# Optimization experiments

Hardware: AMD Instinct MI355X
Metric: run time of the kernel (lower is better)

Reference implementation:

```python
import jax, jax.numpy as jnp
import numpy as np

N_NODES = 50000
N_EDGES = 1600000
N_GRAPHS = 64
DIMS = [3, 256, 256, 256]  # in -> hidden -> hidden -> output
BN_EPS = 1e-5


def setup_inputs() -> dict:
    key = jax.random.key(0)
    ks = jax.random.split(key, 32)
    inp = {}
    inp['x'] = jax.random.normal(ks[0], (N_NODES, DIMS[0]), dtype=jnp.float32)
    inp['edge_index'] = jax.random.randint(ks[1], (2, N_EDGES), 0, N_NODES, dtype=jnp.int64)
    inp['batch'] = jnp.sort(jax.random.randint(ks[2], (N_NODES,), 0, N_GRAPHS, dtype=jnp.int64))
    k = 3
    for i in range(3):
        fi, fo = DIMS[i], DIMS[i + 1]
        inp[f'W{i}'] = jax.random.normal(ks[k], (fi, fo), dtype=jnp.float32) / np.sqrt(fi); k += 1
        inp[f'b{i}'] = jnp.zeros((fo,), dtype=jnp.float32)
        inp[f'g{i}'] = jnp.ones((fo,), dtype=jnp.float32)       # BN weight
        inp[f'be{i}'] = jnp.zeros((fo,), dtype=jnp.float32)     # BN bias
        inp[f'm{i}'] = 0.1 * jax.random.normal(ks[k], (fo,), dtype=jnp.float32); k += 1  # running mean
        inp[f'v{i}'] = jax.random.uniform(ks[k], (fo,), dtype=jnp.float32) + 0.5; k += 1  # running var
    return inp


def _gcn_norm(edge_index, n_nodes):
    # add self-loops, compute symmetric normalization (PyG GCNConv gcn_norm)
    loops = jnp.arange(n_nodes, dtype=edge_index.dtype)
    src = jnp.concatenate([edge_index[0], loops])
    dst = jnp.concatenate([edge_index[1], loops])
    deg = jax.ops.segment_sum(jnp.ones_like(dst, dtype=jnp.float32), dst, num_segments=n_nodes)
    dinv = jnp.where(deg > 0, jax.lax.rsqrt(deg), 0.0)
    norm = dinv[src] * dinv[dst]  # [E+N]
    return src, dst, norm


def _gcn_conv(x, W, b, src, dst, norm, n_nodes):
    h = x @ W                                 # [N, out]
    msg = h[src] * norm[:, None]              # gather + edge weight
    out = jax.ops.segment_sum(msg, dst, num_segments=n_nodes)  # scatter-add
    return out + b


def _bn_eval(x, g, be, m, v):
    return (x - m) * jax.lax.rsqrt(v + BN_EPS) * g + be


def _denan(x):
    return jnp.where(jnp.isnan(x), 0.0, x)


def reference(x, edge_index, batch,
              W0, b0, g0, be0, m0, v0,
              W1, b1, g1, be1, m1, v1,
              W2, b2, g2, be2, m2, v2):
    n = x.shape[0]
    src, dst, norm = _gcn_norm(edge_index, n)
    params = [(W0, b0, g0, be0, m0, v0), (W1, b1, g1, be1, m1, v1), (W2, b2, g2, be2, m2, v2)]
    h = x
    for i, (W, b, g, be, m, v) in enumerate(params):
        h = _gcn_conv(h, W, b, src, dst, norm, n)
        h = _bn_eval(h, g, be, m, v)
        if i < 2:
            h = jax.nn.relu(h)  # dropout is identity in eval mode
        h = _denan(h)
    # global_mean_pool over batch segments
    sums = jax.ops.segment_sum(h, batch, num_segments=N_GRAPHS)
    cnt = jax.ops.segment_sum(jnp.ones((n,), dtype=h.dtype), batch, num_segments=N_GRAPHS)
    out = sums / jnp.maximum(cnt, 1.0)[:, None]
    return _denan(out)
```

## Files before the change

### kernel.cpp

```cpp
#include <hip/hip_runtime.h>

#define NFEAT 256
#define BN_EPSF 1e-5f
#define CH_J 512
#define ELLW 96
#define BSH 7
#define PBKT 392
#define PCAP 4608
#define PEDG 4992
#define W1_SCALE 8.0f
#define Y_DESCALE 0.125f

typedef __attribute__((ext_vector_type(8))) short bf16x8;
typedef __attribute__((ext_vector_type(4))) float f32x4;
typedef __attribute__((ext_vector_type(2))) float f32x2;

__device__ __forceinline__ unsigned short f2bf(float f) {
    union { float f; unsigned u; } v; v.f = f;
    unsigned r = v.u + 0x7fffu + ((v.u >> 16) & 1u);
    return (unsigned short)(r >> 16);
}
__device__ __forceinline__ float bf2f(unsigned short h) {
    union { unsigned u; float f; } v; v.u = ((unsigned)h) << 16;
    return v.f;
}


__global__ __launch_bounds__(256) void k_part(const int* __restrict__ src, const int* __restrict__ dst,
                                              int* __restrict__ curD, int* __restrict__ curS,
                                              unsigned* __restrict__ partD, unsigned* __restrict__ partS, int E) {
    __shared__ int cD[PBKT], cS[PBKT], bD[PBKT], bS[PBKT];
    __shared__ int2 eds[PEDG];
    for (int t = threadIdx.x; t < PBKT; t += 256) { cD[t] = 0; cS[t] = 0; }
    __syncthreads();
    int e0 = blockIdx.x * PEDG;
    int ne = min(E - e0, PEDG);
    for (int i = threadIdx.x; i < ne; i += 256) {
        int2 e; e.x = src[e0 + i]; e.y = dst[e0 + i];
        eds[i] = e;
        atomicAdd(&cD[e.y >> BSH], 1);
        atomicAdd(&cS[e.x >> BSH], 1);
    }
    __syncthreads();
    for (int t = threadIdx.x; t < PBKT; t += 256) {
        bD[t] = cD[t] ? atomicAdd(&curD[t], cD[t]) : 0;
        bS[t] = cS[t] ? atomicAdd(&curS[t], cS[t]) : 0;
        cD[t] = 0; cS[t] = 0;
    }
    __syncthreads();
    for (int i = threadIdx.x; i < ne; i += 256) {
        int2 e = eds[i];
        int b1 = e.y >> BSH;
        int p1 = bD[b1] + atomicAdd(&cD[b1], 1);
        if (p1 < PCAP) partD[(size_t)b1 * PCAP + p1] = ((unsigned)(e.y & 127) << 16) | (unsigned)e.x;
        int b2 = e.x >> BSH;
        int p2 = bS[b2] + atomicAdd(&cS[b2], 1);
        if (p2 < PCAP) partS[(size_t)b2 * PCAP + p2] = ((unsigned)(e.x & 127) << 16) | (unsigned)e.y;
    }
}

__global__ __launch_bounds__(256) void k_prep(const float* __restrict__ W,
                                              unsigned char* __restrict__ Wt_hi, unsigned char* __restrict__ Wt_lo,
                                              const float* __restrict__ x, float4* __restrict__ x4, int N) {
    if (blockIdx.x < 256) {
        int n = blockIdx.x, k = threadIdx.x;
        float w8 = W[k * 256 + n] * W1_SCALE;
        int ph = __builtin_amdgcn_cvt_pk_fp8_f32(w8, w8, 0, false);
        f32x2 dec = __builtin_amdgcn_cvt_pk_f32_fp8(ph, false);
        int pl = __builtin_amdgcn_cvt_pk_fp8_f32(w8 - dec[0], w8 - dec[0], 0, false);
        Wt_hi[n * 256 + k] = (unsigned char)(ph & 0xff);
        Wt_lo[n * 256 + k] = (unsigned char)(pl & 0xff);
    } else {
        int i = (blockIdx.x - 256) * 256 + threadIdx.x;
        if (i < N) {
            float4 r; r.x = x[i * 3 + 0]; r.y = x[i * 3 + 1]; r.z = x[i * 3 + 2]; r.w = 0.f;
            x4[i] = r;
        }
    }
}

__global__ __launch_bounds__(256) void k_buildIn(const unsigned* __restrict__ partD, const int* __restrict__ curD,
                                                 const int* __restrict__ batch,
                                                 unsigned short* __restrict__ ell_in, int* __restrict__ cnt,
                                                 float* __restrict__ dinv, float2* __restrict__ pack, int N) {
    __shared__ int rows[128][ELLW];
    __shared__ int cur[128];
    int b = blockIdx.x;
    if (threadIdx.x < 128) cur[threadIdx.x] = 0;
    __syncthreads();
    int lo = b << BSH;
    int ne = min(curD[b], PCAP);
    const unsigned* seg = partD + (size_t)b * PCAP;
    for (int i = threadIdx.x; i < ne; i += 256) {
        unsigned u = seg[i];
        int r = u >> 16;
        int pos = atomicAdd(&cur[r], 1);
        if (pos < ELLW) rows[r][pos] = (int)(u & 0xFFFFu);
    }
    __syncthreads();
    const int Q = ELLW / 8;
    for (int idx = threadIdx.x; idx < 128 * Q; idx += 256) {
        int r = idx / Q, q = idx % Q;
        if (lo + r < N) {
            unsigned short tmp[8];
#pragma unroll
            for (int j = 0; j < 8; j++) tmp[j] = (unsigned short)rows[r][q * 8 + j];
            *(uint4*)(ell_in + (size_t)(lo + r) * ELLW + q * 8) = *(const uint4*)tmp;
        }
    }
    if (threadIdx.x < 128) {
        int node = lo + threadIdx.x;
        if (node < N) {
            int c = cur[threadIdx.x];
            cnt[node] = c;
            float d = rsqrtf((float)(min(c, ELLW) + 1));
            dinv[node] = d;
            float2 pk; pk.x = d; pk.y = __int_as_float(batch[node]);
            pack[node] = pk;
        }
    }
}

__global__ __launch_bounds__(256) void k_buildCt(const unsigned* __restrict__ partS, const int* __restrict__ curS,
                                                 const float2* __restrict__ pack,
                                                 unsigned short* __restrict__ ct_hi,
                                                 unsigned short* __restrict__ ct_lo,
                                                 int N, int N_pad) {
    __shared__ float ct[128][65];
    __shared__ float dv[128];
    int b = blockIdx.x;
    for (int idx = threadIdx.x; idx < 128 * 65; idx += 256) (&ct[0][0])[idx] = 0.f;
    __syncthreads();
    int lo = b << BSH;
    int ne = min(curS[b], PCAP);
    const unsigned* seg = partS + (size_t)b * PCAP;
    for (int i = threadIdx.x; i < ne; i += 256) {
        unsigned u = seg[i];
        float2 pk = pack[u & 0xFFFFu];
        atomicAdd(&ct[u >> 16][__float_as_int(pk.y)], pk.x);
    }
    __syncthreads();
    if (threadIdx.x < 128) {
        int node = lo + threadIdx.x;
        if (node < N) {
            float2 ps = pack[node];
            dv[threadIdx.x] = ps.x;
            ct[threadIdx.x][__float_as_int(ps.y)] += ps.x;
        } else dv[threadIdx.x] = 0.f;
    }
    __syncthreads();
    int g = threadIdx.x >> 2, js = (threadIdx.x & 3) * 32;
    unsigned short hv[32], lv[32];
#pragma unroll
    for (int j = 0; j < 32; j++) {
        float val = dv[js + j] * ct[js + j][g];
        unsigned short h = f2bf(val);
        hv[j] = h;
        lv[j] = f2bf(val - bf2f(h));
    }
    size_t basep = (size_t)g * N_pad + lo + js;
#pragma unroll
    for (int j = 0; j < 32; j += 8) {
        *(uint4*)(ct_hi + basep + j) = *(const uint4*)&hv[j];
        *(uint4*)(ct_lo + basep + j) = *(const uint4*)&lv[j];
    }
}


__global__ __launch_bounds__(256) void k_l0(const float4* __restrict__ x4, const unsigned short* __restrict__ ell_in,
                                            const int* __restrict__ cnt, const float* __restrict__ dinv,
                                            const float* __restrict__ W, const float* __restrict__ b,
                                            const float* __restrict__ g, const float* __restrict__ be,
                                            const float* __restrict__ m, const float* __restrict__ v,
                                            unsigned char* __restrict__ h8, int N) {
    int wv = threadIdx.x >> 6, lane = threadIdx.x & 63;
    int node = blockIdx.x * 4 + wv;
    int c4 = lane * 4;
    if (node >= N) {
        *(unsigned*)(h8 + (size_t)node * NFEAT + c4) = 0u;
        return;
    }
    float dvn = dinv[node];
    int len = min(cnt[node], ELLW);
    const unsigned short* nb = ell_in + (size_t)node * ELLW;
    float a0 = 0.f, a1 = 0.f, a2 = 0.f;
    for (int e = lane; e < len; e += 64) {
        int s = nb[e];
        float4 xv = x4[s];
        float w = dinv[s] * dvn;
        a0 += w * xv.x;
        a1 += w * xv.y;
        a2 += w * xv.z;
    }
#pragma unroll
    for (int off = 32; off; off >>= 1) {
        a0 += __shfl_xor(a0, off);
        a1 += __shfl_xor(a1, off);
        a2 += __shfl_xor(a2, off);
    }
    float4 xs = x4[node];
    float wself = dvn * dvn;
    a0 += wself * xs.x;
    a1 += wself * xs.y;
    a2 += wself * xs.z;
    float4 w0 = *(const float4*)(W + c4);
    float4 w1 = *(const float4*)(W + NFEAT + c4);
    float4 w2 = *(const float4*)(W + 2 * NFEAT + c4);
    float4 bb = *(const float4*)(b + c4);
    float4 gg = *(const float4*)(g + c4);
    float4 ee = *(const float4*)(be + c4);
    float4 mm = *(const float4*)(m + c4);
    float4 vv = *(const float4*)(v + c4);
    float r0 = ((a0 * w0.x + a1 * w1.x + a2 * w2.x) + bb.x - mm.x) * rsqrtf(vv.x + BN_EPSF) * gg.x + ee.x;
    float r1 = ((a0 * w0.y + a1 * w1.y + a2 * w2.y) + bb.y - mm.y) * rsqrtf(vv.y + BN_EPSF) * gg.y + ee.y;
    float r2 = ((a0 * w0.z + a1 * w1.z + a2 * w2.z) + bb.z - mm.z) * rsqrtf(vv.z + BN_EPSF) * gg.z + ee.z;
    float r3 = ((a0 * w0.w + a1 * w1.w + a2 * w2.w) + bb.w - mm.w) * rsqrtf(vv.w + BN_EPSF) * gg.w + ee.w;
    r0 = fmaxf(r0, 0.f); r1 = fmaxf(r1, 0.f); r2 = fmaxf(r2, 0.f); r3 = fmaxf(r3, 0.f);
    int p01 = __builtin_amdgcn_cvt_pk_fp8_f32(r0, r1, 0, false);
    int p23 = __builtin_amdgcn_cvt_pk_fp8_f32(r2, r3, 0, false);
    unsigned pk = (unsigned)(p01 & 0xffff) | ((unsigned)(p23 & 0xffff) << 16);
    *(unsigned*)(h8 + (size_t)node * NFEAT + c4) = pk;
}


__global__ __launch_bounds__(256) void k_mm_mfma(const unsigned char* __restrict__ A8,
                                                 const unsigned char* __restrict__ Bh,
                                                 const unsigned char* __restrict__ Bl,
                                                 unsigned char* __restrict__ C8) {
    __shared__ __align__(16) unsigned char As[4][128][8];
    __shared__ __align__(16) unsigned char Bhs[4][128][8];
    __shared__ __align__(16) unsigned char Bls[4][128][8];
    int bm = blockIdx.x * 128, bn = blockIdx.y * 128;
    int tid = threadIdx.x;
    int lane = tid & 63, wave = tid >> 6;
    int wm = (wave & 1) * 64, wn = (wave >> 1) * 64;
    int lrow = lane & 15, lk = lane >> 4;
    f32x4 acc[4][4] = {};

    for (int k0 = 0; k0 < 256; k0 += 32) {
#pragma unroll
        for (int i = 0; i < 2; i++) {
            int idx = tid + 256 * i;
            int ch = idx & 3, row = idx >> 2;
            *(uint2*)(&As[ch][row][0])  = *(const uint2*)(A8 + (size_t)(bm + row) * 256 + k0 + ch * 8);
            *(uint2*)(&Bhs[ch][row][0]) = *(const uint2*)(Bh + (size_t)(bn + row) * 256 + k0 + ch * 8);
            *(uint2*)(&Bls[ch][row][0]) = *(const uint2*)(Bl + (size_t)(bn + row) * 256 + k0 + ch * 8);
        }
        __syncthreads();
        long af[4], bh[4], bl[4];
#pragma unroll
        for (int r = 0; r < 4; r++) af[r] = *(const long*)(&As[lk][wm + r * 16 + lrow][0]);
#pragma unroll
        for (int c = 0; c < 4; c++) {
            bh[c] = *(const long*)(&Bhs[lk][wn + c * 16 + lrow][0]);
            bl[c] = *(const long*)(&Bls[lk][wn + c * 16 + lrow][0]);
        }
#pragma unroll
        for (int r = 0; r < 4; r++)
#pragma unroll
            for (int c = 0; c < 4; c++) {
                acc[r][c] = __builtin_amdgcn_mfma_f32_16x16x32_fp8_fp8(af[r], bh[c], acc[r][c], 0, 0, 0);
                acc[r][c] = __builtin_amdgcn_mfma_f32_16x16x32_fp8_fp8(af[r], bl[c], acc[r][c], 0, 0, 0);
            }
        __syncthreads();
    }

#pragma unroll
    for (int r = 0; r < 4; r++) {
#pragma unroll
        for (int reg = 0; reg < 4; reg++) {
            int grow = bm + wm + r * 16 + lk * 4 + reg;
            int p01 = __builtin_amdgcn_cvt_pk_fp8_f32(acc[r][0][reg], acc[r][1][reg], 0, false);
            int p23 = __builtin_amdgcn_cvt_pk_fp8_f32(acc[r][2][reg], acc[r][3][reg], 0, false);
            size_t base = (size_t)grow * 256 + bn + wn + lrow;
            C8[base]      = (unsigned char)(p01 & 0xff);
            C8[base + 16] = (unsigned char)((p01 >> 8) & 0xff);
            C8[base + 32] = (unsigned char)(p23 & 0xff);
            C8[base + 48] = (unsigned char)((p23 >> 8) & 0xff);
        }
    }
}


template <bool RELU>
__global__ __launch_bounds__(64) void k_agg256b(const unsigned char* __restrict__ t,
                                                const unsigned short* __restrict__ ell_in,
                                                const int* __restrict__ cnt,
                                                const float* __restrict__ dinv,
                                                const float* __restrict__ b, const float* __restrict__ g,
                                                const float* __restrict__ be, const float* __restrict__ m,
                                                const float* __restrict__ v, unsigned short* __restrict__ out, int N) {
    __shared__ int s_idx[64];
    __shared__ float s_w[64];
    int node = blockIdx.x;
    int c4 = threadIdx.x * 4;
    if (node >= N) {
        ushort4 z = {0, 0, 0, 0};
        *(ushort4*)(out + (size_t)node * NFEAT + c4) = z;
        return;
    }
    float dv = dinv[node];
    float a0, a1, a2, a3;
    {
        unsigned u = *(const unsigned*)(t + (size_t)node * NFEAT + c4);
        f32x2 flo = __builtin_amdgcn_cvt_pk_f32_fp8(u, false);
        f32x2 fhi = __builtin_amdgcn_cvt_pk_f32_fp8(u, true);
        float w = dv * dv;
        a0 = w * flo[0]; a1 = w * flo[1]; a2 = w * fhi[0]; a3 = w * fhi[1];
    }
    int len = min(cnt[node], ELLW);
    const unsigned short* nb = ell_in + (size_t)node * ELLW;
    for (int base = 0; base < len; base += 64) {
        int chunk = min(64, len - base);
        if ((int)threadIdx.x < chunk) {
            int s = nb[base + threadIdx.x];
            s_idx[threadIdx.x] = s;
            s_w[threadIdx.x] = dinv[s] * dv;
        }
        __syncthreads();
        int j = 0;
        for (; j + 4 <= chunk; j += 4) {
            unsigned u0 = *(const unsigned*)(t + (size_t)s_idx[j + 0] * NFEAT + c4);
            unsigned u1 = *(const unsigned*)(t + (size_t)s_idx[j + 1] * NFEAT + c4);
            unsigned u2 = *(const unsigned*)(t + (size_t)s_idx[j + 2] * NFEAT + c4);
            unsigned u3 = *(const unsigned*)(t + (size_t)s_idx[j + 3] * NFEAT + c4);
            float w0 = s_w[j + 0], w1 = s_w[j + 1], w2 = s_w[j + 2], w3 = s_w[j + 3];
            f32x2 l0 = __builtin_amdgcn_cvt_pk_f32_fp8(u0, false), h0 = __builtin_amdgcn_cvt_pk_f32_fp8(u0, true);
            f32x2 l1 = __builtin_amdgcn_cvt_pk_f32_fp8(u1, false), h1 = __builtin_amdgcn_cvt_pk_f32_fp8(u1, true);
            f32x2 l2 = __builtin_amdgcn_cvt_pk_f32_fp8(u2, false), h2 = __builtin_amdgcn_cvt_pk_f32_fp8(u2, true);
            f32x2 l3 = __builtin_amdgcn_cvt_pk_f32_fp8(u3, false), h3 = __builtin_amdgcn_cvt_pk_f32_fp8(u3, true);
            a0 += w0 * l0[0]; a1 += w0 * l0[1]; a2 += w0 * h0[0]; a3 += w0 * h0[1];
            a0 += w1 * l1[0]; a1 += w1 * l1[1]; a2 += w1 * h1[0]; a3 += w1 * h1[1];
            a0 += w2 * l2[0]; a1 += w2 * l2[1]; a2 += w2 * h2[0]; a3 += w2 * h2[1];
            a0 += w3 * l3[0]; a1 += w3 * l3[1]; a2 += w3 * h3[0]; a3 += w3 * h3[1];
        }
        for (; j < chunk; j++) {
            unsigned u = *(const unsigned*)(t + (size_t)s_idx[j] * NFEAT + c4);
            float w = s_w[j];
            f32x2 flo = __builtin_amdgcn_cvt_pk_f32_fp8(u, false);
            f32x2 fhi = __builtin_amdgcn_cvt_pk_f32_fp8(u, true);
            a0 += w * flo[0]; a1 += w * flo[1]; a2 += w * fhi[0]; a3 += w * fhi[1];
        }
        __syncthreads();
    }
    a0 *= Y_DESCALE; a1 *= Y_DESCALE; a2 *= Y_DESCALE; a3 *= Y_DESCALE;
    float4 bb = *(const float4*)(b + c4);
    float4 gg = *(const float4*)(g + c4);
    float4 ee = *(const float4*)(be + c4);
    float4 mm = *(const float4*)(m + c4);
    float4 vv = *(const float4*)(v + c4);
    float r0 = (a0 + bb.x - mm.x) * rsqrtf(vv.x + BN_EPSF) * gg.x + ee.x;
    float r1 = (a1 + bb.y - mm.y) * rsqrtf(vv.y + BN_EPSF) * gg.y + ee.y;
    float r2 = (a2 + bb.z - mm.z) * rsqrtf(vv.z + BN_EPSF) * gg.z + ee.z;
    float r3 = (a3 + bb.w - mm.w) * rsqrtf(vv.w + BN_EPSF) * gg.w + ee.w;
    if (RELU) { r0 = fmaxf(r0, 0.f); r1 = fmaxf(r1, 0.f); r2 = fmaxf(r2, 0.f); r3 = fmaxf(r3, 0.f); }
    ushort4 o; o.x = f2bf(r0); o.y = f2bf(r1); o.z = f2bf(r2); o.w = f2bf(r3);
    *(ushort4*)(out + (size_t)node * NFEAT + c4) = o;
}


__global__ __launch_bounds__(256) void k_cgemm(const unsigned short* __restrict__ Y,
                                               const unsigned short* __restrict__ ct_hi,
                                               const unsigned short* __restrict__ ct_lo,
                                               float* __restrict__ P, int N_pad) {
    __shared__ __align__(16) unsigned short s_hi[64 * 40];
    __shared__ __align__(16) unsigned short s_lo[64 * 40];
    int tid = threadIdx.x;
    int lane = tid & 63, wv = tid >> 6;
    int lc = lane & 15, q = lane >> 4;
    int cbase = blockIdx.y * 64 + wv * 16;
    int j0 = blockIdx.x * CH_J;
    int sg = tid >> 2, sj8 = (tid & 3) * 8;
    f32x4 acc[4] = {};

    for (int ks = 0; ks < CH_J; ks += 32) {
        size_t cbs = (size_t)sg * N_pad + j0 + ks + sj8;
        *(uint4*)(&s_hi[sg * 40 + sj8]) = *(const uint4*)(ct_hi + cbs);
        *(uint4*)(&s_lo[sg * 40 + sj8]) = *(const uint4*)(ct_lo + cbs);
        __syncthreads();
        const unsigned short* yp = Y + (size_t)(j0 + ks + q * 8) * 256 + cbase + lc;
        bf16x8 a;
#pragma unroll
        for (int jj = 0; jj < 8; jj++) a[jj] = (short)yp[(size_t)jj * 256];
#pragma unroll
        for (int nt = 0; nt < 4; nt++) {
            bf16x8 bh = *(const bf16x8*)(&s_hi[(nt * 16 + lc) * 40 + q * 8]);
            bf16x8 bl = *(const bf16x8*)(&s_lo[(nt * 16 + lc) * 40 + q * 8]);
            acc[nt] = __builtin_amdgcn_mfma_f32_16x16x32_bf16(a, bh, acc[nt], 0, 0, 0);
            acc[nt] = __builtin_amdgcn_mfma_f32_16x16x32_bf16(a, bl, acc[nt], 0, 0, 0);
        }
        __syncthreads();
    }
    float* pp = P + (size_t)blockIdx.x * 64 * 256;
#pragma unroll
    for (int nt = 0; nt < 4; nt++) {
        int g = nt * 16 + lc;
#pragma unroll
        for (int reg = 0; reg < 4; reg++) {
            int c = cbase + q * 4 + reg;
            pp[(size_t)c * 64 + g] = acc[nt][reg];
        }
    }
}

__global__ __launch_bounds__(64) void k_redP(const float* __restrict__ P,
                                             float* __restrict__ pooled, int nch) {
    int c = blockIdx.x;
    int g = threadIdx.x;
    float acc = 0.f;
    const float* pp = P + (size_t)c * 64 + g;
    for (int ch = 0; ch < nch; ch++) acc += pp[(size_t)ch * 64 * 256];
    pooled[(size_t)g * 256 + c] = acc;
}

__global__ __launch_bounds__(256) void k_out(const float* __restrict__ pooled,
                                             const float* __restrict__ W2,
                                             const int* __restrict__ batch,
                                             const float* __restrict__ b, const float* __restrict__ gw,
                                             const float* __restrict__ be, const float* __restrict__ m,
                                             const float* __restrict__ v,
                                             float* __restrict__ out, int N) {
    __shared__ float s_pool[256];
    __shared__ int s_cnt;
    int g = blockIdx.x;
    int c = threadIdx.x;
    s_pool[c] = pooled[(size_t)g * 256 + c];
    if (threadIdx.x == 0) {
        int lo = 0, hi = N;
        while (lo < hi) { int mid = (lo + hi) >> 1; if (batch[mid] < g) lo = mid + 1; else hi = mid; }
        int st = lo;
        lo = 0; hi = N;
        while (lo < hi) { int mid = (lo + hi) >> 1; if (batch[mid] < g + 1) lo = mid + 1; else hi = mid; }
        s_cnt = lo - st;
    }
    __syncthreads();
    float dot = 0.f;
    for (int k = 0; k < 256; k += 4) {
        float4 pk = *(const float4*)(s_pool + k);
        dot += pk.x * W2[(k + 0) * 256 + c];
        dot += pk.y * W2[(k + 1) * 256 + c];
        dot += pk.z * W2[(k + 2) * 256 + c];
        dot += pk.w * W2[(k + 3) * 256 + c];
    }
    float r = 0.f;
    int cntg = s_cnt;
    if (cntg > 0) {
        float mean = dot / (float)cntg + b[c];
        r = (mean - m[c]) * rsqrtf(v[c] + BN_EPSF) * gw[c] + be[c];
    }
    out[g * 256 + c] = r;
}


static inline size_t align_up(size_t x, size_t a) { return (x + a - 1) & ~(a - 1); }

extern "C" void kernel_launch(void* const* d_in, const int* in_sizes, int n_in,
                              void* d_out, int out_size, void* d_ws, size_t ws_size,
                              hipStream_t stream) {
    const float* x = (const float*)d_in[0];
    const int* edge_index = (const int*)d_in[1];
    const int* batch = (const int*)d_in[2];

    const int N = in_sizes[2];
    const int E = in_sizes[1] / 2;
    const int NCH = (N + CH_J - 1) / CH_J;
    const int N_pad = NCH * CH_J;

    const int* e_src = edge_index;
    const int* e_dst = edge_index + E;

    const float* W[3]; const float* bP[3]; const float* gP[3];
    const float* beP[3]; const float* mP[3]; const float* vP[3];
    for (int i = 0; i < 3; i++) {
        W[i]  = (const float*)d_in[3 + 6 * i + 0];
        bP[i] = (const float*)d_in[3 + 6 * i + 1];
        gP[i] = (const float*)d_in[3 + 6 * i + 2];
        beP[i]= (const float*)d_in[3 + 6 * i + 3];
        mP[i] = (const float*)d_in[3 + 6 * i + 4];
        vP[i] = (const float*)d_in[3 + 6 * i + 5];
    }

    char* ws = (char*)d_ws;
    size_t off = 0;
    auto carve = [&](size_t bytes) { void* p = ws + off; off = align_up(off + bytes, 256); return p; };
    int*   curD     = (int*)  carve((size_t)2 * PBKT * 4);
    int*   curS     = curD + PBKT;
    int*   cnt      = (int*)  carve((size_t)N * 4);
    float* dinv     = (float*)carve((size_t)N * 4);
    float2* pack    = (float2*)carve((size_t)N * 8);
    float4* x4      = (float4*)carve((size_t)N * 16);
    unsigned* partD = (unsigned*)carve((size_t)PBKT * PCAP * 4);
    unsigned* partS = (unsigned*)carve((size_t)PBKT * PCAP * 4);
    unsigned short* ell_in = (unsigned short*)carve((size_t)N * ELLW * 2);
    unsigned short* bufA = (unsigned short*)carve((size_t)N_pad * NFEAT * 2);
    unsigned char*  bufA0 = (unsigned char*)carve((size_t)N_pad * NFEAT);
    unsigned char*  bufY = (unsigned char*)carve((size_t)N_pad * NFEAT);
    unsigned char*  Wt_hi = (unsigned char*)carve((size_t)NFEAT * NFEAT);
    unsigned char*  Wt_lo = (unsigned char*)carve((size_t)NFEAT * NFEAT);
    unsigned short* ct_hi = (unsigned short*)carve((size_t)N_pad * 64 * 2);
    unsigned short* ct_lo = (unsigned short*)carve((size_t)N_pad * 64 * 2);
    float* partials = (float*)carve((size_t)NCH * 64 * 256 * 4);
    float* pooled   = (float*)carve((size_t)64 * 256 * 4);
    (void)ws_size;

    hipMemsetAsync(curD, 0, (size_t)2 * PBKT * 4, stream);

    const int BS = 256;
    k_part<<<(E + PEDG - 1) / PEDG, BS, 0, stream>>>(e_src, e_dst, curD, curS, partD, partS, E);
    k_prep<<<256 + (N + BS - 1) / BS, BS, 0, stream>>>(W[1], Wt_hi, Wt_lo, x, x4, N);
    k_buildIn<<<PBKT, BS, 0, stream>>>(partD, curD, batch, ell_in, cnt, dinv, pack, N);
    k_buildCt<<<PBKT, BS, 0, stream>>>(partS, curS, pack, ct_hi, ct_lo, N, N_pad);

    k_l0<<<N_pad / 4, BS, 0, stream>>>(x4, ell_in, cnt, dinv, W[0],
                                       bP[0], gP[0], beP[0], mP[0], vP[0], bufA0, N);

    dim3 mmGrid((N + 127) / 128, 2);
    k_mm_mfma<<<mmGrid, 256, 0, stream>>>(bufA0, Wt_hi, Wt_lo, bufY);
    k_agg256b<true><<<N_pad, 64, 0, stream>>>(bufY, ell_in, cnt, dinv,
                                              bP[1], gP[1], beP[1], mP[1], vP[1], bufA, N);

    dim3 cgGrid(NCH, 4);
    k_cgemm<<<cgGrid, 256, 0, stream>>>(bufA, ct_hi, ct_lo, partials, N_pad);
    k_redP<<<256, 64, 0, stream>>>(partials, pooled, NCH);
    k_out<<<64, 256, 0, stream>>>(pooled, W[2], batch, bP[2], gP[2], beP[2], mP[2], vP[2],
                                  (float*)d_out, N);
}
```

Measured before the change: 324.9 us.

## Pack four nodes per block in aggregation with scalar indices and packed FMA

The layer-1 aggregation kernel now runs four wavefronts per 256-thread block, one node each, instead of one 64-thread block per node. Neighbor index and weight are packed as int2 in shared memory and broadcast through readfirstlane, so the gather addresses come from scalar registers. The inner loop is unrolled to 8 gathers with packed f32x2 FMAs. This cuts block-launch overhead and exposes more memory-level parallelism. In exchange, all four waves loop to the block's maximum chunk count with block-wide barriers, so a short-degree node waits on its longest sibling.

New measurement: 333.3 us. +2.6%, slower.

```diff
diff --git a/kernel.cpp b/kernel.cpp
--- a/kernel.cpp
+++ b/kernel.cpp
@@ -282,68 +282,116 @@
 }
 
 
+__device__ __forceinline__ f32x2 pk_fma2(f32x2 x, float w, f32x2 acc) {
+    f32x2 ww = {w, w};
+    return x * ww + acc;
+}
+
 template <bool RELU>
-__global__ __launch_bounds__(64) void k_agg256b(const unsigned char* __restrict__ t,
-                                                const unsigned short* __restrict__ ell_in,
-                                                const int* __restrict__ cnt,
-                                                const float* __restrict__ dinv,
-                                                const float* __restrict__ b, const float* __restrict__ g,
-                                                const float* __restrict__ be, const float* __restrict__ m,
-                                                const float* __restrict__ v, unsigned short* __restrict__ out, int N) {
-    __shared__ int s_idx[64];
-    __shared__ float s_w[64];
-    int node = blockIdx.x;
-    int c4 = threadIdx.x * 4;
-    if (node >= N) {
-        ushort4 z = {0, 0, 0, 0};
-        *(ushort4*)(out + (size_t)node * NFEAT + c4) = z;
-        return;
-    }
-    float dv = dinv[node];
-    float a0, a1, a2, a3;
-    {
+__global__ __launch_bounds__(256) void k_agg256b(const unsigned char* __restrict__ t,
+                                                 const unsigned short* __restrict__ ell_in,
+                                                 const int* __restrict__ cnt,
+                                                 const float* __restrict__ dinv,
+                                                 const float* __restrict__ b, const float* __restrict__ g,
+                                                 const float* __restrict__ be, const float* __restrict__ m,
+                                                 const float* __restrict__ v, unsigned short* __restrict__ out, int N) {
+    __shared__ int2 s_sw[4][64];
+    __shared__ int s_nch;
+    int wv = threadIdx.x >> 6, lane = threadIdx.x & 63;
+    int node = blockIdx.x * 4 + wv;
+    int c4 = lane * 4;
+    bool valid = node < N;
+    float dv = valid ? dinv[node] : 0.f;
+    int len = valid ? min(cnt[node], ELLW) : 0;
+    if (threadIdx.x == 0) s_nch = 0;
+    __syncthreads();
+    if (lane == 0 && len > 0) atomicMax(&s_nch, (len + 63) >> 6);
+
+    f32x2 aLo = {0.f, 0.f}, aHi = {0.f, 0.f};
+    if (valid) {
         unsigned u = *(const unsigned*)(t + (size_t)node * NFEAT + c4);
         f32x2 flo = __builtin_amdgcn_cvt_pk_f32_fp8(u, false);
         f32x2 fhi = __builtin_amdgcn_cvt_pk_f32_fp8(u, true);
         float w = dv * dv;
-        a0 = w * flo[0]; a1 = w * flo[1]; a2 = w * fhi[0]; a3 = w * fhi[1];
-    }
-    int len = min(cnt[node], ELLW);
+        aLo = pk_fma2(flo, w, aLo);
+        aHi = pk_fma2(fhi, w, aHi);
+    }
+    __syncthreads();
+    int nch = s_nch;
     const unsigned short* nb = ell_in + (size_t)node * ELLW;
-    for (int base = 0; base < len; base += 64) {
-        int chunk = min(64, len - base);
-        if ((int)threadIdx.x < chunk) {
-            int s = nb[base + threadIdx.x];
-            s_idx[threadIdx.x] = s;
-            s_w[threadIdx.x] = dinv[s] * dv;
+
+    for (int it = 0; it < nch; ++it) {
+        int base = it << 6;
+        int chunk = min(len - base, 64);
+        if (lane < chunk) {
+            int s = nb[base + lane];
+            int2 p; p.x = s; p.y = __float_as_int(dinv[s] * dv);
+            s_sw[wv][lane] = p;
         }
         __syncthreads();
         int j = 0;
-        for (; j + 4 <= chunk; j += 4) {
-            unsigned u0 = *(const unsigned*)(t + (size_t)s_idx[j + 0] * NFEAT + c4);
-            unsigned u1 = *(const unsigned*)(t + (size_t)s_idx[j + 1] * NFEAT + c4);
-            unsigned u2 = *(const unsigned*)(t + (size_t)s_idx[j + 2] * NFEAT + c4);
-            unsigned u3 = *(const unsigned*)(t + (size_t)s_idx[j + 3] * NFEAT + c4);
-            float w0 = s_w[j + 0], w1 = s_w[j + 1], w2 = s_w[j + 2], w3 = s_w[j + 3];
-            f32x2 l0 = __builtin_amdgcn_cvt_pk_f32_fp8(u0, false), h0 = __builtin_amdgcn_cvt_pk_f32_fp8(u0, true);
-            f32x2 l1 = __builtin_amdgcn_cvt_pk_f32_fp8(u1, false), h1 = __builtin_amdgcn_cvt_pk_f32_fp8(u1, true);
-            f32x2 l2 = __builtin_amdgcn_cvt_pk_f32_fp8(u2, false), h2 = __builtin_amdgcn_cvt_pk_f32_fp8(u2, true);
-            f32x2 l3 = __builtin_amdgcn_cvt_pk_f32_fp8(u3, false), h3 = __builtin_amdgcn_cvt_pk_f32_fp8(u3, true);
-            a0 += w0 * l0[0]; a1 += w0 * l0[1]; a2 += w0 * h0[0]; a3 += w0 * h0[1];
-            a0 += w1 * l1[0]; a1 += w1 * l1[1]; a2 += w1 * h1[0]; a3 += w1 * h1[1];
-            a0 += w2 * l2[0]; a1 += w2 * l2[1]; a2 += w2 * h2[0]; a3 += w2 * h2[1];
-            a0 += w3 * l3[0]; a1 += w3 * l3[1]; a2 += w3 * h3[0]; a3 += w3 * h3[1];
+        for (; j + 8 <= chunk; j += 8) {
+            int2 p0 = s_sw[wv][j + 0], p1 = s_sw[wv][j + 1], p2 = s_sw[wv][j + 2], p3 = s_sw[wv][j + 3];
+            int2 p4 = s_sw[wv][j + 4], p5 = s_sw[wv][j + 5], p6 = s_sw[wv][j + 6], p7 = s_sw[wv][j + 7];
+            int s0 = __builtin_amdgcn_readfirstlane(p0.x);
+            int s1 = __builtin_amdgcn_readfirstlane(p1.x);
+            int s2 = __builtin_amdgcn_readfirstlane(p2.x);
+            int s3 = __builtin_amdgcn_readfirstlane(p3.x);
+            int s4 = __builtin_amdgcn_readfirstlane(p4.x);
+            int s5 = __builtin_amdgcn_readfirstlane(p5.x);
+            int s6 = __builtin_amdgcn_readfirstlane(p6.x);
+            int s7 = __builtin_amdgcn_readfirstlane(p7.x);
+            unsigned u0 = *(const unsigned*)(t + (size_t)s0 * NFEAT + c4);
+            unsigned u1 = *(const unsigned*)(t + (size_t)s1 * NFEAT + c4);
+            unsigned u2 = *(const unsigned*)(t + (size_t)s2 * NFEAT + c4);
+            unsigned u3 = *(const unsigned*)(t + (size_t)s3 * NFEAT + c4);
+            unsigned u4 = *(const unsigned*)(t + (size_t)s4 * NFEAT + c4);
+            unsigned u5 = *(const unsigned*)(t + (size_t)s5 * NFEAT + c4);
+            unsigned u6 = *(const unsigned*)(t + (size_t)s6 * NFEAT + c4);
+            unsigned u7 = *(const unsigned*)(t + (size_t)s7 * NFEAT + c4);
+            float w0 = __uint_as_float(__builtin_amdgcn_readfirstlane(p0.y));
+            float w1 = __uint_as_float(__builtin_amdgcn_readfirstlane(p1.y));
+            float w2 = __uint_as_float(__builtin_amdgcn_readfirstlane(p2.y));
+            float w3 = __uint_as_float(__builtin_amdgcn_readfirstlane(p3.y));
+            float w4 = __uint_as_float(__builtin_amdgcn_readfirstlane(p4.y));
+            float w5 = __uint_as_float(__builtin_amdgcn_readfirstlane(p5.y));
+            float w6 = __uint_as_float(__builtin_amdgcn_readfirstlane(p6.y));
+            float w7 = __uint_as_float(__builtin_amdgcn_readfirstlane(p7.y));
+            aLo = pk_fma2(__builtin_amdgcn_cvt_pk_f32_fp8(u0, false), w0, aLo);
+            aHi = pk_fma2(__builtin_amdgcn_cvt_pk_f32_fp8(u0, true),  w0, aHi);
+            aLo = pk_fma2(__builtin_amdgcn_cvt_pk_f32_fp8(u1, false), w1, aLo);
+            aHi = pk_fma2(__builtin_amdgcn_cvt_pk_f32_fp8(u1, true),  w1, aHi);
+            aLo = pk_fma2(__builtin_amdgcn_cvt_pk_f32_fp8(u2, false), w2, aLo);
+            aHi = pk_fma2(__builtin_amdgcn_cvt_pk_f32_fp8(u2, true),  w2, aHi);
+            aLo = pk_fma2(__builtin_amdgcn_cvt_pk_f32_fp8(u3, false), w3, aLo);
+            aHi = pk_fma2(__builtin_amdgcn_cvt_pk_f32_fp8(u3, true),  w3, aHi);
+            aLo = pk_fma2(__builtin_amdgcn_cvt_pk_f32_fp8(u4, false), w4, aLo);
+            aHi = pk_fma2(__builtin_amdgcn_cvt_pk_f32_fp8(u4, true),  w4, aHi);
+            aLo = pk_fma2(__builtin_amdgcn_cvt_pk_f32_fp8(u5, false), w5, aLo);
+            aHi = pk_fma2(__builtin_amdgcn_cvt_pk_f32_fp8(u5, true),  w5, aHi);
+            aLo = pk_fma2(__builtin_amdgcn_cvt_pk_f32_fp8(u6, false), w6, aLo);
+            aHi = pk_fma2(__builtin_amdgcn_cvt_pk_f32_fp8(u6, true),  w6, aHi);
+            aLo = pk_fma2(__builtin_amdgcn_cvt_pk_f32_fp8(u7, false), w7, aLo);
+            aHi = pk_fma2(__builtin_amdgcn_cvt_pk_f32_fp8(u7, true),  w7, aHi);
         }
         for (; j < chunk; j++) {
-            unsigned u = *(const unsigned*)(t + (size_t)s_idx[j] * NFEAT + c4);
-            float w = s_w[j];
-            f32x2 flo = __builtin_amdgcn_cvt_pk_f32_fp8(u, false);
-            f32x2 fhi = __builtin_amdgcn_cvt_pk_f32_fp8(u, true);
-            a0 += w * flo[0]; a1 += w * flo[1]; a2 += w * fhi[0]; a3 += w * fhi[1];
+            int2 p = s_sw[wv][j];
+            int s = __builtin_amdgcn_readfirstlane(p.x);
+            float w = __uint_as_float(__builtin_amdgcn_readfirstlane(p.y));
+            unsigned u = *(const unsigned*)(t + (size_t)s * NFEAT + c4);
+            aLo = pk_fma2(__builtin_amdgcn_cvt_pk_f32_fp8(u, false), w, aLo);
+            aHi = pk_fma2(__builtin_amdgcn_cvt_pk_f32_fp8(u, true),  w, aHi);
         }
         __syncthreads();
     }
-    a0 *= Y_DESCALE; a1 *= Y_DESCALE; a2 *= Y_DESCALE; a3 *= Y_DESCALE;
+
+    if (!valid) {
+        ushort4 z = {0, 0, 0, 0};
+        *(ushort4*)(out + (size_t)node * NFEAT + c4) = z;
+        return;
+    }
+    float a0 = aLo[0] * Y_DESCALE, a1 = aLo[1] * Y_DESCALE;
+    float a2 = aHi[0] * Y_DESCALE, a3 = aHi[1] * Y_DESCALE;
     float4 bb = *(const float4*)(b + c4);
     float4 gg = *(const float4*)(g + c4);
     float4 ee = *(const float4*)(be + c4);
@@ -516,8 +564,8 @@
 
     dim3 mmGrid((N + 127) / 128, 2);
     k_mm_mfma<<<mmGrid, 256, 0, stream>>>(bufA0, Wt_hi, Wt_lo, bufY);
-    k_agg256b<true><<<N_pad, 64, 0, stream>>>(bufY, ell_in, cnt, dinv,
-                                              bP[1], gP[1], beP[1], mP[1], vP[1], bufA, N);
+    k_agg256b<true><<<N_pad / 4, 256, 0, stream>>>(bufY, ell_in, cnt, dinv,
+                                                   bP[1], gP[1], beP[1], mP[1], vP[1], bufA, N);
 
     dim3 cgGrid(NCH, 4);
     k_cgemm<<<cgGrid, 256, 0, stream>>>(bufA, ct_hi, ct_lo, partials, N_pad);
```

## Fuse independent kernels, fold source dinv into GEMM epilogue, merge pooling reduction

Applied to the files above, without the earlier changes.

Merges the edge partitioning and weight/x prep into one launch, and the transpose-count build and layer-0 aggregation into another, using block-index ranges. The GEMM epilogue now pre-scales each row by its dinv, so the layer-1 aggregation only sums fp8 neighbor rows without per-edge weight lookups. The aggregation loop is unrolled by 8 with 32-bit offsets. The partials reduction is folded into k_out with vectorised partial stores, which removes several launches. Pre-scaling before fp8 quantisation changes rounding, and the kernel now mixes heterogeneous block types.

Result: faster. 315.2 us (-3.0%).

```diff
diff --git a/kernel.cpp b/kernel.cpp
--- a/kernel.cpp
+++ b/kernel.cpp
@@ -26,11 +26,34 @@
 }
 
 
-__global__ __launch_bounds__(256) void k_part(const int* __restrict__ src, const int* __restrict__ dst,
-                                              int* __restrict__ curD, int* __restrict__ curS,
-                                              unsigned* __restrict__ partD, unsigned* __restrict__ partS, int E) {
+__global__ __launch_bounds__(256) void k_part_prep(const int* __restrict__ src, const int* __restrict__ dst,
+                                                   int* __restrict__ curD, int* __restrict__ curS,
+                                                   unsigned* __restrict__ partD, unsigned* __restrict__ partS,
+                                                   int E, int NPB,
+                                                   const float* __restrict__ W1,
+                                                   unsigned char* __restrict__ Wt_hi, unsigned char* __restrict__ Wt_lo,
+                                                   const float* __restrict__ x, float4* __restrict__ x4, int N) {
     __shared__ int cD[PBKT], cS[PBKT], bD[PBKT], bS[PBKT];
     __shared__ int2 eds[PEDG];
+    if ((int)blockIdx.x >= NPB) {
+        int bx = (int)blockIdx.x - NPB;
+        if (bx < 256) {
+            int n = bx, k = threadIdx.x;
+            float w8 = W1[k * 256 + n] * W1_SCALE;
+            int ph = __builtin_amdgcn_cvt_pk_fp8_f32(w8, w8, 0, false);
+            f32x2 dec = __builtin_amdgcn_cvt_pk_f32_fp8(ph, false);
+            int pl = __builtin_amdgcn_cvt_pk_fp8_f32(w8 - dec[0], w8 - dec[0], 0, false);
+            Wt_hi[n * 256 + k] = (unsigned char)(ph & 0xff);
+            Wt_lo[n * 256 + k] = (unsigned char)(pl & 0xff);
+        } else {
+            int i = (bx - 256) * 256 + threadIdx.x;
+            if (i < N) {
+                float4 r; r.x = x[i * 3 + 0]; r.y = x[i * 3 + 1]; r.z = x[i * 3 + 2]; r.w = 0.f;
+                x4[i] = r;
+            }
+        }
+        return;
+    }
     for (int t = threadIdx.x; t < PBKT; t += 256) { cD[t] = 0; cS[t] = 0; }
     __syncthreads();
     int e0 = blockIdx.x * PEDG;
@@ -56,26 +79,6 @@
         int b2 = e.x >> BSH;
         int p2 = bS[b2] + atomicAdd(&cS[b2], 1);
         if (p2 < PCAP) partS[(size_t)b2 * PCAP + p2] = ((unsigned)(e.x & 127) << 16) | (unsigned)e.y;
-    }
-}
-
-__global__ __launch_bounds__(256) void k_prep(const float* __restrict__ W,
-                                              unsigned char* __restrict__ Wt_hi, unsigned char* __restrict__ Wt_lo,
-                                              const float* __restrict__ x, float4* __restrict__ x4, int N) {
-    if (blockIdx.x < 256) {
-        int n = blockIdx.x, k = threadIdx.x;
-        float w8 = W[k * 256 + n] * W1_SCALE;
-        int ph = __builtin_amdgcn_cvt_pk_fp8_f32(w8, w8, 0, false);
-        f32x2 dec = __builtin_amdgcn_cvt_pk_f32_fp8(ph, false);
-        int pl = __builtin_amdgcn_cvt_pk_fp8_f32(w8 - dec[0], w8 - dec[0], 0, false);
-        Wt_hi[n * 256 + k] = (unsigned char)(ph & 0xff);
-        Wt_lo[n * 256 + k] = (unsigned char)(pl & 0xff);
-    } else {
-        int i = (blockIdx.x - 256) * 256 + threadIdx.x;
-        if (i < N) {
-            float4 r; r.x = x[i * 3 + 0]; r.y = x[i * 3 + 1]; r.z = x[i * 3 + 2]; r.w = 0.f;
-            x4[i] = r;
-        }
     }
 }
 
@@ -121,63 +124,63 @@
     }
 }
 
-__global__ __launch_bounds__(256) void k_buildCt(const unsigned* __restrict__ partS, const int* __restrict__ curS,
-                                                 const float2* __restrict__ pack,
-                                                 unsigned short* __restrict__ ct_hi,
-                                                 unsigned short* __restrict__ ct_lo,
-                                                 int N, int N_pad) {
+
+__global__ __launch_bounds__(256) void k_bct_l0(const unsigned* __restrict__ partS, const int* __restrict__ curS,
+                                                const float2* __restrict__ pack,
+                                                unsigned short* __restrict__ ct_hi,
+                                                unsigned short* __restrict__ ct_lo,
+                                                const float4* __restrict__ x4, const unsigned short* __restrict__ ell_in,
+                                                const int* __restrict__ cnt, const float* __restrict__ dinv,
+                                                const float* __restrict__ W, const float* __restrict__ b,
+                                                const float* __restrict__ g, const float* __restrict__ be,
+                                                const float* __restrict__ m, const float* __restrict__ v,
+                                                unsigned char* __restrict__ h8, int N, int N_pad) {
     __shared__ float ct[128][65];
     __shared__ float dv[128];
-    int b = blockIdx.x;
-    for (int idx = threadIdx.x; idx < 128 * 65; idx += 256) (&ct[0][0])[idx] = 0.f;
-    __syncthreads();
-    int lo = b << BSH;
-    int ne = min(curS[b], PCAP);
-    const unsigned* seg = partS + (size_t)b * PCAP;
-    for (int i = threadIdx.x; i < ne; i += 256) {
-        unsigned u = seg[i];
-        float2 pk = pack[u & 0xFFFFu];
-        atomicAdd(&ct[u >> 16][__float_as_int(pk.y)], pk.x);
-    }
-    __syncthreads();
-    if (threadIdx.x < 128) {
-        int node = lo + threadIdx.x;
-        if (node < N) {
-            float2 ps = pack[node];
-            dv[threadIdx.x] = ps.x;
-            ct[threadIdx.x][__float_as_int(ps.y)] += ps.x;
-        } else dv[threadIdx.x] = 0.f;
-    }
-    __syncthreads();
-    int g = threadIdx.x >> 2, js = (threadIdx.x & 3) * 32;
-    unsigned short hv[32], lv[32];
-#pragma unroll
-    for (int j = 0; j < 32; j++) {
-        float val = dv[js + j] * ct[js + j][g];
-        unsigned short h = f2bf(val);
-        hv[j] = h;
-        lv[j] = f2bf(val - bf2f(h));
-    }
-    size_t basep = (size_t)g * N_pad + lo + js;
-#pragma unroll
-    for (int j = 0; j < 32; j += 8) {
-        *(uint4*)(ct_hi + basep + j) = *(const uint4*)&hv[j];
-        *(uint4*)(ct_lo + basep + j) = *(const uint4*)&lv[j];
-    }
-}
-
-
-__global__ __launch_bounds__(256) void k_l0(const float4* __restrict__ x4, const unsigned short* __restrict__ ell_in,
-                                            const int* __restrict__ cnt, const float* __restrict__ dinv,
-                                            const float* __restrict__ W, const float* __restrict__ b,
-                                            const float* __restrict__ g, const float* __restrict__ be,
-                                            const float* __restrict__ m, const float* __restrict__ v,
-                                            unsigned char* __restrict__ h8, int N) {
+    if (blockIdx.x < PBKT) {
+        int bq = blockIdx.x;
+        for (int idx = threadIdx.x; idx < 128 * 65; idx += 256) (&ct[0][0])[idx] = 0.f;
+        __syncthreads();
+        int lo = bq << BSH;
+        int ne = min(curS[bq], PCAP);
+        const unsigned* seg = partS + (size_t)bq * PCAP;
+        for (int i = threadIdx.x; i < ne; i += 256) {
+            unsigned u = seg[i];
+            float2 pk = pack[u & 0xFFFFu];
+            atomicAdd(&ct[u >> 16][__float_as_int(pk.y)], pk.x);
+        }
+        __syncthreads();
+        if (threadIdx.x < 128) {
+            int node = lo + threadIdx.x;
+            if (node < N) {
+                float2 ps = pack[node];
+                dv[threadIdx.x] = ps.x;
+                ct[threadIdx.x][__float_as_int(ps.y)] += ps.x;
+            } else dv[threadIdx.x] = 0.f;
+        }
+        __syncthreads();
+        int gq = threadIdx.x >> 2, js = (threadIdx.x & 3) * 32;
+        unsigned short hv[32], lv[32];
+#pragma unroll
+        for (int j = 0; j < 32; j++) {
+            float val = dv[js + j] * ct[js + j][gq];
+            unsigned short h = f2bf(val);
+            hv[j] = h;
+            lv[j] = f2bf(val - bf2f(h));
+        }
+        size_t basep = (size_t)gq * N_pad + lo + js;
+#pragma unroll
+        for (int j = 0; j < 32; j += 8) {
+            *(uint4*)(ct_hi + basep + j) = *(const uint4*)&hv[j];
+            *(uint4*)(ct_lo + basep + j) = *(const uint4*)&lv[j];
+        }
+        return;
+    }
     int wv = threadIdx.x >> 6, lane = threadIdx.x & 63;
-    int node = blockIdx.x * 4 + wv;
+    int node = ((int)blockIdx.x - PBKT) * 4 + wv;
     int c4 = lane * 4;
     if (node >= N) {
-        *(unsigned*)(h8 + (size_t)node * NFEAT + c4) = 0u;
+        if (node < N_pad) *(unsigned*)(h8 + (size_t)node * NFEAT + c4) = 0u;
         return;
     }
     float dvn = dinv[node];
@@ -226,7 +229,8 @@
 __global__ __launch_bounds__(256) void k_mm_mfma(const unsigned char* __restrict__ A8,
                                                  const unsigned char* __restrict__ Bh,
                                                  const unsigned char* __restrict__ Bl,
-                                                 unsigned char* __restrict__ C8) {
+                                                 const float* __restrict__ dinv,
+                                                 unsigned char* __restrict__ C8, int N) {
     __shared__ __align__(16) unsigned char As[4][128][8];
     __shared__ __align__(16) unsigned char Bhs[4][128][8];
     __shared__ __align__(16) unsigned char Bls[4][128][8];
@@ -270,8 +274,9 @@
 #pragma unroll
         for (int reg = 0; reg < 4; reg++) {
             int grow = bm + wm + r * 16 + lk * 4 + reg;
-            int p01 = __builtin_amdgcn_cvt_pk_fp8_f32(acc[r][0][reg], acc[r][1][reg], 0, false);
-            int p23 = __builtin_amdgcn_cvt_pk_fp8_f32(acc[r][2][reg], acc[r][3][reg], 0, false);
+            float dn = (grow < N) ? dinv[grow] : 0.f;
+            int p01 = __builtin_amdgcn_cvt_pk_fp8_f32(acc[r][0][reg] * dn, acc[r][1][reg] * dn, 0, false);
+            int p23 = __builtin_amdgcn_cvt_pk_fp8_f32(acc[r][2][reg] * dn, acc[r][3][reg] * dn, 0, false);
             size_t base = (size_t)grow * 256 + bn + wn + lrow;
             C8[base]      = (unsigned char)(p01 & 0xff);
             C8[base + 16] = (unsigned char)((p01 >> 8) & 0xff);
@@ -283,15 +288,14 @@
 
 
 template <bool RELU>
-__global__ __launch_bounds__(64) void k_agg256b(const unsigned char* __restrict__ t,
-                                                const unsigned short* __restrict__ ell_in,
-                                                const int* __restrict__ cnt,
-                                                const float* __restrict__ dinv,
-                                                const float* __restrict__ b, const float* __restrict__ g,
-                                                const float* __restrict__ be, const float* __restrict__ m,
-                                                const float* __restrict__ v, unsigned short* __restrict__ out, int N) {
-    __shared__ int s_idx[64];
-    __shared__ float s_w[64];
+__global__ __launch_bounds__(64) void k_agg2(const unsigned char* __restrict__ t,
+                                             const unsigned short* __restrict__ ell_in,
+                                             const int* __restrict__ cnt,
+                                             const float* __restrict__ dinv,
+                                             const float* __restrict__ b, const float* __restrict__ g,
+                                             const float* __restrict__ be, const float* __restrict__ m,
+                                             const float* __restrict__ v, unsigned short* __restrict__ out, int N) {
+    __shared__ int s_off[64];
     int node = blockIdx.x;
     int c4 = threadIdx.x * 4;
     if (node >= N) {
@@ -299,51 +303,58 @@
         *(ushort4*)(out + (size_t)node * NFEAT + c4) = z;
         return;
     }
-    float dv = dinv[node];
-    float a0, a1, a2, a3;
+    const unsigned char* tp = t;
+    f32x2 aLo, aHi;
     {
-        unsigned u = *(const unsigned*)(t + (size_t)node * NFEAT + c4);
-        f32x2 flo = __builtin_amdgcn_cvt_pk_f32_fp8(u, false);
-        f32x2 fhi = __builtin_amdgcn_cvt_pk_f32_fp8(u, true);
-        float w = dv * dv;
-        a0 = w * flo[0]; a1 = w * flo[1]; a2 = w * fhi[0]; a3 = w * fhi[1];
+        unsigned u = *(const unsigned*)(tp + (unsigned)((node << 8) + c4));
+        aLo = __builtin_amdgcn_cvt_pk_f32_fp8(u, false);
+        aHi = __builtin_amdgcn_cvt_pk_f32_fp8(u, true);
     }
     int len = min(cnt[node], ELLW);
     const unsigned short* nb = ell_in + (size_t)node * ELLW;
     for (int base = 0; base < len; base += 64) {
         int chunk = min(64, len - base);
-        if ((int)threadIdx.x < chunk) {
-            int s = nb[base + threadIdx.x];
-            s_idx[threadIdx.x] = s;
-            s_w[threadIdx.x] = dinv[s] * dv;
-        }
+        if ((int)threadIdx.x < chunk)
+            s_off[threadIdx.x] = ((int)nb[base + threadIdx.x]) << 8;
         __syncthreads();
         int j = 0;
-        for (; j + 4 <= chunk; j += 4) {
-            unsigned u0 = *(const unsigned*)(t + (size_t)s_idx[j + 0] * NFEAT + c4);
-            unsigned u1 = *(const unsigned*)(t + (size_t)s_idx[j + 1] * NFEAT + c4);
-            unsigned u2 = *(const unsigned*)(t + (size_t)s_idx[j + 2] * NFEAT + c4);
-            unsigned u3 = *(const unsigned*)(t + (size_t)s_idx[j + 3] * NFEAT + c4);
-            float w0 = s_w[j + 0], w1 = s_w[j + 1], w2 = s_w[j + 2], w3 = s_w[j + 3];
-            f32x2 l0 = __builtin_amdgcn_cvt_pk_f32_fp8(u0, false), h0 = __builtin_amdgcn_cvt_pk_f32_fp8(u0, true);
-            f32x2 l1 = __builtin_amdgcn_cvt_pk_f32_fp8(u1, false), h1 = __builtin_amdgcn_cvt_pk_f32_fp8(u1, true);
-            f32x2 l2 = __builtin_amdgcn_cvt_pk_f32_fp8(u2, false), h2 = __builtin_amdgcn_cvt_pk_f32_fp8(u2, true);
-            f32x2 l3 = __builtin_amdgcn_cvt_pk_f32_fp8(u3, false), h3 = __builtin_amdgcn_cvt_pk_f32_fp8(u3, true);
-            a0 += w0 * l0[0]; a1 += w0 * l0[1]; a2 += w0 * h0[0]; a3 += w0 * h0[1];
-            a0 += w1 * l1[0]; a1 += w1 * l1[1]; a2 += w1 * h1[0]; a3 += w1 * h1[1];
-            a0 += w2 * l2[0]; a1 += w2 * l2[1]; a2 += w2 * h2[0]; a3 += w2 * h2[1];
-            a0 += w3 * l3[0]; a1 += w3 * l3[1]; a2 += w3 * h3[0]; a3 += w3 * h3[1];
+        for (; j + 8 <= chunk; j += 8) {
+            int o0 = s_off[j + 0], o1 = s_off[j + 1], o2 = s_off[j + 2], o3 = s_off[j + 3];
+            int o4 = s_off[j + 4], o5 = s_off[j + 5], o6 = s_off[j + 6], o7 = s_off[j + 7];
+            unsigned u0 = *(const unsigned*)(tp + (unsigned)(o0 + c4));
+            unsigned u1 = *(const unsigned*)(tp + (unsigned)(o1 + c4));
+            unsigned u2 = *(const unsigned*)(tp + (unsigned)(o2 + c4));
+            unsigned u3 = *(const unsigned*)(tp + (unsigned)(o3 + c4));
+            unsigned u4 = *(const unsigned*)(tp + (unsigned)(o4 + c4));
+            unsigned u5 = *(const unsigned*)(tp + (unsigned)(o5 + c4));
+            unsigned u6 = *(const unsigned*)(tp + (unsigned)(o6 + c4));
+            unsigned u7 = *(const unsigned*)(tp + (unsigned)(o7 + c4));
+            aLo = aLo + __builtin_amdgcn_cvt_pk_f32_fp8(u0, false);
+            aHi = aHi + __builtin_amdgcn_cvt_pk_f32_fp8(u0, true);
+            aLo = aLo + __builtin_amdgcn_cvt_pk_f32_fp8(u1, false);
+            aHi = aHi + __builtin_amdgcn_cvt_pk_f32_fp8(u1, true);
+            aLo = aLo + __builtin_amdgcn_cvt_pk_f32_fp8(u2, false);
+            aHi = aHi + __builtin_amdgcn_cvt_pk_f32_fp8(u2, true);
+            aLo = aLo + __builtin_amdgcn_cvt_pk_f32_fp8(u3, false);
+            aHi = aHi + __builtin_amdgcn_cvt_pk_f32_fp8(u3, true);
+            aLo = aLo + __builtin_amdgcn_cvt_pk_f32_fp8(u4, false);
+            aHi = aHi + __builtin_amdgcn_cvt_pk_f32_fp8(u4, true);
+            aLo = aLo + __builtin_amdgcn_cvt_pk_f32_fp8(u5, false);
+            aHi = aHi + __builtin_amdgcn_cvt_pk_f32_fp8(u5, true);
+            aLo = aLo + __builtin_amdgcn_cvt_pk_f32_fp8(u6, false);
+            aHi = aHi + __builtin_amdgcn_cvt_pk_f32_fp8(u6, true);
+            aLo = aLo + __builtin_amdgcn_cvt_pk_f32_fp8(u7, false);
+            aHi = aHi + __builtin_amdgcn_cvt_pk_f32_fp8(u7, true);
         }
         for (; j < chunk; j++) {
-            unsigned u = *(const unsigned*)(t + (size_t)s_idx[j] * NFEAT + c4);
-            float w = s_w[j];
-            f32x2 flo = __builtin_amdgcn_cvt_pk_f32_fp8(u, false);
-            f32x2 fhi = __builtin_amdgcn_cvt_pk_f32_fp8(u, true);
-            a0 += w * flo[0]; a1 += w * flo[1]; a2 += w * fhi[0]; a3 += w * fhi[1];
-        }
-        __syncthreads();
-    }
-    a0 *= Y_DESCALE; a1 *= Y_DESCALE; a2 *= Y_DESCALE; a3 *= Y_DESCALE;
+            unsigned u = *(const unsigned*)(tp + (unsigned)(s_off[j] + c4));
+            aLo = aLo + __builtin_amdgcn_cvt_pk_f32_fp8(u, false);
+            aHi = aHi + __builtin_amdgcn_cvt_pk_f32_fp8(u, true);
+        }
+        __syncthreads();
+    }
+    float s = dinv[node] * Y_DESCALE;
+    float a0 = aLo[0] * s, a1 = aLo[1] * s, a2 = aHi[0] * s, a3 = aHi[1] * s;
     float4 bb = *(const float4*)(b + c4);
     float4 gg = *(const float4*)(g + c4);
     float4 ee = *(const float4*)(be + c4);
@@ -394,26 +405,13 @@
     float* pp = P + (size_t)blockIdx.x * 64 * 256;
 #pragma unroll
     for (int nt = 0; nt < 4; nt++) {
-        int g = nt * 16 + lc;
-#pragma unroll
-        for (int reg = 0; reg < 4; reg++) {
-            int c = cbase + q * 4 + reg;
-            pp[(size_t)c * 64 + g] = acc[nt][reg];
-        }
-    }
-}
-
-__global__ __launch_bounds__(64) void k_redP(const float* __restrict__ P,
-                                             float* __restrict__ pooled, int nch) {
-    int c = blockIdx.x;
-    int g = threadIdx.x;
-    float acc = 0.f;
-    const float* pp = P + (size_t)c * 64 + g;
-    for (int ch = 0; ch < nch; ch++) acc += pp[(size_t)ch * 64 * 256];
-    pooled[(size_t)g * 256 + c] = acc;
-}
-
-__global__ __launch_bounds__(256) void k_out(const float* __restrict__ pooled,
+        int gq = nt * 16 + lc;
+        *(f32x4*)(pp + (size_t)gq * 256 + cbase + q * 4) = acc[nt];
+    }
+}
+
+
+__global__ __launch_bounds__(256) void k_out(const float* __restrict__ P, int nch,
                                              const float* __restrict__ W2,
                                              const int* __restrict__ batch,
                                              const float* __restrict__ b, const float* __restrict__ gw,
@@ -424,7 +422,10 @@
     __shared__ int s_cnt;
     int g = blockIdx.x;
     int c = threadIdx.x;
-    s_pool[c] = pooled[(size_t)g * 256 + c];
+    float acc = 0.f;
+    const float* pp = P + (size_t)g * 256 + c;
+    for (int ch = 0; ch < nch; ch++) acc += pp[(size_t)ch * 64 * 256];
+    s_pool[c] = acc;
     if (threadIdx.x == 0) {
         int lo = 0, hi = N;
         while (lo < hi) { int mid = (lo + hi) >> 1; if (batch[mid] < g) lo = mid + 1; else hi = mid; }
@@ -500,28 +501,25 @@
     unsigned short* ct_hi = (unsigned short*)carve((size_t)N_pad * 64 * 2);
     unsigned short* ct_lo = (unsigned short*)carve((size_t)N_pad * 64 * 2);
     float* partials = (float*)carve((size_t)NCH * 64 * 256 * 4);
-    float* pooled   = (float*)carve((size_t)64 * 256 * 4);
     (void)ws_size;
 
     hipMemsetAsync(curD, 0, (size_t)2 * PBKT * 4, stream);
 
     const int BS = 256;
-    k_part<<<(E + PEDG - 1) / PEDG, BS, 0, stream>>>(e_src, e_dst, curD, curS, partD, partS, E);
-    k_prep<<<256 + (N + BS - 1) / BS, BS, 0, stream>>>(W[1], Wt_hi, Wt_lo, x, x4, N);
+    const int NPB = (E + PEDG - 1) / PEDG;
+
+    k_part_prep<<<NPB + 256 + (N + BS - 1) / BS, BS, 0, stream>>>(
+        e_src, e_dst, curD, curS, partD, partS, E, NPB, W[1], Wt_hi, Wt_lo, x, x4, N);
     k_buildIn<<<PBKT, BS, 0, stream>>>(partD, curD, batch, ell_in, cnt, dinv, pack, N);
-    k_buildCt<<<PBKT, BS, 0, stream>>>(partS, curS, pack, ct_hi, ct_lo, N, N_pad);
-
-    k_l0<<<N_pad / 4, BS, 0, stream>>>(x4, ell_in, cnt, dinv, W[0],
-                                       bP[0], gP[0], beP[0], mP[0], vP[0], bufA0, N);
-
+    k_bct_l0<<<PBKT + N_pad / 4, BS, 0, stream>>>(partS, curS, pack, ct_hi, ct_lo,
+                                                  x4, ell_in, cnt, dinv, W[0],
+                                                  bP[0], gP[0], beP[0], mP[0], vP[0], bufA0, N, N_pad);
     dim3 mmGrid((N + 127) / 128, 2);
-    k_mm_mfma<<<mmGrid, 256, 0, stream>>>(bufA0, Wt_hi, Wt_lo, bufY);
-    k_agg256b<true><<<N_pad, 64, 0, stream>>>(bufY, ell_in, cnt, dinv,
-                                              bP[1], gP[1], beP[1], mP[1], vP[1], bufA, N);
-
+    k_mm_mfma<<<mmGrid, 256, 0, stream>>>(bufA0, Wt_hi, Wt_lo, dinv, bufY, N);
+    k_agg2<true><<<N_pad, 64, 0, stream>>>(bufY, ell_in, cnt, dinv,
+                                           bP[1], gP[1], beP[1], mP[1], vP[1], bufA, N);
     dim3 cgGrid(NCH, 4);
     k_cgemm<<<cgGrid, 256, 0, stream>>>(bufA, ct_hi, ct_lo, partials, N_pad);
-    k_redP<<<256, 64, 0, stream>>>(partials, pooled, NCH);
-    k_out<<<64, 256, 0, stream>>>(pooled, W[2], batch, bP[2], gP[2], beP[2], mP[2], vP[2],
+    k_out<<<64, 256, 0, stream>>>(partials, NCH, W[2], batch, bP[2], gP[2], beP[2], mP[2], vP[2],
                                   (float*)d_out, N);
 }
```
